# Kernel tuning notes

Hardware: AMD Instinct MI355X
Metric: run time of the kernel (lower is better)

Reference implementation:

```python
import jax, jax.numpy as jnp
import numpy as np

B, NIN, DIN, M, DOUT = 256, 64, 128, 32, 128
SCALE = 1.0 / np.sqrt(DOUT)  # 1/sqrt(out_d_capsules)


def setup_inputs() -> dict:
    key = jax.random.key(0)
    k1, k2, k3 = jax.random.split(key, 3)
    w_const = float(np.sqrt(M / (DIN * NIN)))  # weight_init_const
    return {
        "x": jax.random.normal(k1, (B, NIN, DIN), dtype=jnp.float32),
        "current_act": jax.random.uniform(k2, (B, NIN), dtype=jnp.float32),
        "W": w_const * jax.random.normal(k3, (NIN, DIN, M, DOUT), dtype=jnp.float32),
        "num_iter": 3,
    }


def reference(x, current_act, W, num_iter):
    # Initial pass: next_capsule_value is None -> q0 = softmax(zeros) = 1/M uniform
    # einsum('nm,bna,namd->bmd', q0, x, W) with uniform q0 == mean over m-weighting = /M
    ncv = jnp.einsum('bna,namd->bmd', x, W) / M  # [B, M, Dout]
    q = jnp.full((B, NIN, M), 1.0 / M, dtype=x.dtype)  # query_key from init step
    # Routing iterations (act_type='EM' -> next_act is None; dp=0 -> no dropout)
    for _ in range(max(1, num_iter)):
        logits = jnp.einsum('bna,namd,bmd->bnm', x, W, ncv) * SCALE  # [B, Nin, M]
        q = jax.nn.softmax(logits, axis=2)
        ncv = jnp.einsum('bnm,bna,namd,bn->bmd', q, x, W, current_act)
    # Per-pair votes and routed class embeddings
    votes = jnp.einsum('bna,namd->bnmd', x, W)          # [B, Nin, M, Dout]
    weights = q * current_act[:, :, None]               # [B, Nin, M]
    route_class_emb = weights[..., None] * votes        # [B, Nin, M, Dout]
    return ncv, q, route_class_emb
```

## Files before the change

kernel.cpp:

```cpp
#include <hip/hip_runtime.h>
#include <math.h>

#define B_    256
#define NIN_  64
#define DIN_  128
#define M_    32
#define DOUT_ 128
#define NUM_ITER 3

static constexpr float SCALE = 0.0883883476483184405501f;

typedef __attribute__((ext_vector_type(8))) short bf16x8;
typedef __attribute__((ext_vector_type(4))) float f32x4;

__device__ __forceinline__ unsigned short f2bf(float f) {
    union { float f; unsigned u; } c; c.f = f;
    unsigned r = c.u + 0x7FFFu + ((c.u >> 16) & 1u);
    return (unsigned short)(r >> 16);
}
__device__ __forceinline__ float lo2f(unsigned u) {
    union { unsigned u; float f; } c; c.u = u << 16; return c.f;
}
__device__ __forceinline__ float hi2f(unsigned u) {
    union { unsigned u; float f; } c; c.u = u & 0xffff0000u; return c.f;
}


__global__ __launch_bounds__(256) void k_votes_mfma(const float* __restrict__ x,
                                                    const float* __restrict__ W,
                                                    float* __restrict__ route) {
    const int n    = blockIdx.x;
    const int j0   = blockIdx.y * 512;
    const int t    = threadIdx.x;
    const int w    = t >> 6;
    const int lane = t & 63;
    const int l15  = lane & 15;
    const int l4   = lane >> 4;

    __shared__ __align__(16) char lds[49152];
    char* xbuf = lds;
    char* wbuf = lds + 32768;

    bf16x8 af[4][4];

    for (int h = 0; h < 2; ++h) {
        {
            const int col4 = (t & 15) * 4;
            const int roff = t >> 4;
            const int boff = col4 * 2;
            for (int p = 0; p < 16; ++p) {
                int row = p * 16 + roff;
                const float* src = x + (size_t)row * (NIN_ * DIN_) + (size_t)n * DIN_ + h * 64 + col4;
                float4 v = *(const float4*)src;
                uint2 pk;
                pk.x = (unsigned)f2bf(v.x) | ((unsigned)f2bf(v.y) << 16);
                pk.y = (unsigned)f2bf(v.z) | ((unsigned)f2bf(v.w) << 16);
                *(uint2*)(xbuf + row * 128 + (boff ^ ((row & 7) << 4))) = pk;
            }
        }
        __syncthreads();
#pragma unroll
        for (int mf = 0; mf < 4; ++mf) {
            int row = w * 64 + mf * 16 + l15;
            int sw  = (row & 7) << 4;
#pragma unroll
            for (int kfh = 0; kfh < 2; ++kfh) {
                int kbyte = kfh * 64 + l4 * 16;
                af[mf][h * 2 + kfh] = *(const bf16x8*)(xbuf + row * 128 + (kbyte ^ sw));
            }
        }
        __syncthreads();
    }

    const int jlane = t & 63;
    const int kg    = t >> 6;

    for (int jt = 0; jt < 8; ++jt) {
        {
            const int jcol = j0 + jt * 64 + jlane;
            const float* Wp = W + (size_t)n * (DIN_ * M_ * DOUT_) + jcol;
            const int sw = (jlane & 7) << 4;
#pragma unroll
            for (int c = 0; c < 4; ++c) {
                int kbase = kg * 32 + c * 8;
                unsigned pk[4];
#pragma unroll
                for (int r = 0; r < 4; ++r) {
                    float f0 = Wp[(size_t)(kbase + 2 * r)     * 4096];
                    float f1 = Wp[(size_t)(kbase + 2 * r + 1) * 4096];
                    pk[r] = (unsigned)f2bf(f0) | ((unsigned)f2bf(f1) << 16);
                }
                *(uint4*)(wbuf + jlane * 256 + ((kbase * 2) ^ sw)) = *(uint4*)pk;
            }
        }
        __syncthreads();

        f32x4 acc[4][4];
#pragma unroll
        for (int mf = 0; mf < 4; ++mf)
#pragma unroll
            for (int nf = 0; nf < 4; ++nf) acc[mf][nf] = (f32x4){0.f, 0.f, 0.f, 0.f};

#pragma unroll
        for (int kf = 0; kf < 4; ++kf) {
            bf16x8 bfr[4];
            int kbyte = kf * 64 + l4 * 16;
#pragma unroll
            for (int nf = 0; nf < 4; ++nf) {
                int col = nf * 16 + l15;
                bfr[nf] = *(const bf16x8*)(wbuf + col * 256 + (kbyte ^ ((col & 7) << 4)));
            }
#pragma unroll
            for (int mf = 0; mf < 4; ++mf)
#pragma unroll
                for (int nf = 0; nf < 4; ++nf)
                    acc[mf][nf] = __builtin_amdgcn_mfma_f32_16x16x32_bf16(af[mf][kf], bfr[nf], acc[mf][nf], 0, 0, 0);
        }
        __syncthreads();

#pragma unroll
        for (int mf = 0; mf < 4; ++mf) {
#pragma unroll
            for (int nf = 0; nf < 4; ++nf) {
                const int jb = nf * 16 + l15;
#pragma unroll
                for (int r = 0; r < 4; ++r) {
                    const int b = w * 64 + mf * 16 + l4 * 4 + r;
                    *(unsigned short*)(xbuf + b * 128 + ((jb * 2) ^ ((b & 12) << 3))) = f2bf(acc[mf][nf][r]);
                }
            }
        }
        __syncthreads();

        {
            char* vout = (char*)route;
            const size_t obase = (size_t)524288 + (size_t)n * 8192 + (size_t)(j0 + jt * 64) * 2;
#pragma unroll
            for (int p = 0; p < 8; ++p) {
                const int b = p * 32 + (t >> 3);
                const int c = (t & 7) * 16;
                uint4 val = *(const uint4*)(xbuf + b * 128 + (c ^ ((b & 12) << 3)));
                *(uint4*)(vout + (size_t)b * 1048576 + obase + c) = val;
            }
        }
        __syncthreads();
    }
}

__global__ __launch_bounds__(512, 2) void k_fused(float* __restrict__ route,
                                                  const float* __restrict__ act,
                                                  float* __restrict__ ncv,
                                                  float* __restrict__ q_out) {
    const int b    = blockIdx.x;
    const int t    = threadIdx.x;
    const int base = t * 8;
    const int m    = t >> 4;

    __shared__ float logits_s[4][32];
    __shared__ float w_s[4][32];
    __shared__ float sact[NIN_];
    if (t < 64) sact[t] = act[b * 64 + t];

    const char* vb    = (const char*)route + (size_t)b * 1048576 + 524288;
    const size_t toff = (size_t)t * 16;

    uint4 vA[4], vB[4];
    float ncvp[8], acc[8];

#define LOADC(DST, CC) { \
    _Pragma("unroll") \
    for (int r = 0; r < 4; ++r) \
        DST[r] = *(const uint4*)(vb + (size_t)((CC) * 4 + r) * 8192 + toff); }

#define SUM4(V) { \
    _Pragma("unroll") \
    for (int r = 0; r < 4; ++r) { \
        acc[0] += lo2f(V[r].x); acc[1] += hi2f(V[r].x); \
        acc[2] += lo2f(V[r].y); acc[3] += hi2f(V[r].y); \
        acc[4] += lo2f(V[r].z); acc[5] += hi2f(V[r].z); \
        acc[6] += lo2f(V[r].w); acc[7] += hi2f(V[r].w); } }

#define PH_A(V) { \
    _Pragma("unroll") \
    for (int r = 0; r < 4; ++r) { \
        float p = 0.f; \
        p = fmaf(lo2f(V[r].x), ncvp[0], p); p = fmaf(hi2f(V[r].x), ncvp[1], p); \
        p = fmaf(lo2f(V[r].y), ncvp[2], p); p = fmaf(hi2f(V[r].y), ncvp[3], p); \
        p = fmaf(lo2f(V[r].z), ncvp[4], p); p = fmaf(hi2f(V[r].z), ncvp[5], p); \
        p = fmaf(lo2f(V[r].w), ncvp[6], p); p = fmaf(hi2f(V[r].w), ncvp[7], p); \
        p += __shfl_xor(p, 1); p += __shfl_xor(p, 2); \
        p += __shfl_xor(p, 4); p += __shfl_xor(p, 8); \
        if ((t & 15) == 0) logits_s[r][m] = p * SCALE; \
    } }

#define PH_B(CC, WRF) { \
    if (t < 128) { \
        const int rr = t >> 5; const int ln = t & 31; \
        float l  = logits_s[rr][ln]; \
        float mx = l; \
        mx = fmaxf(mx, __shfl_xor(mx, 1));  mx = fmaxf(mx, __shfl_xor(mx, 2)); \
        mx = fmaxf(mx, __shfl_xor(mx, 4));  mx = fmaxf(mx, __shfl_xor(mx, 8)); \
        mx = fmaxf(mx, __shfl_xor(mx, 16)); \
        float e  = __expf(l - mx); \
        float su = e; \
        su += __shfl_xor(su, 1);  su += __shfl_xor(su, 2); \
        su += __shfl_xor(su, 4);  su += __shfl_xor(su, 8);  su += __shfl_xor(su, 16); \
        float qv = e / su; \
        const int ng = (CC) * 4 + rr; \
        w_s[rr][ln] = qv * sact[ng]; \
        if (WRF) q_out[(size_t)b * 2048 + (size_t)ng * 32 + ln] = qv; \
    } }

#define PH_C(V, CC, WRF) { \
    _Pragma("unroll") \
    for (int r = 0; r < 4; ++r) { \
        const float wg = w_s[r][m]; \
        float f0 = lo2f(V[r].x), f1 = hi2f(V[r].x), f2 = lo2f(V[r].y), f3 = hi2f(V[r].y); \
        float f4 = lo2f(V[r].z), f5 = hi2f(V[r].z), f6 = lo2f(V[r].w), f7 = hi2f(V[r].w); \
        acc[0] = fmaf(wg, f0, acc[0]); acc[1] = fmaf(wg, f1, acc[1]); \
        acc[2] = fmaf(wg, f2, acc[2]); acc[3] = fmaf(wg, f3, acc[3]); \
        acc[4] = fmaf(wg, f4, acc[4]); acc[5] = fmaf(wg, f5, acc[5]); \
        acc[6] = fmaf(wg, f6, acc[6]); acc[7] = fmaf(wg, f7, acc[7]); \
        if (WRF) { \
            float4 r0 = {wg * f0, wg * f1, wg * f2, wg * f3}; \
            float4 r1 = {wg * f4, wg * f5, wg * f6, wg * f7}; \
            float* rp = route + (size_t)b * 262144 + (size_t)((CC) * 4 + r) * 4096 + base; \
            *(float4*)rp = r0; *(float4*)(rp + 4) = r1; \
        } \
    } }

#define PROC(V, CC, WRF) { PH_A(V); __syncthreads(); PH_B(CC, WRF); __syncthreads(); PH_C(V, CC, WRF); }

#define ITER_PASS(WRF, WRAP) { \
    _Pragma("unroll") for (int i = 0; i < 8; ++i) acc[i] = 0.f; \
    LOADC(vB, 1); \
    for (int cc = 0; cc < 16; cc += 2) { \
        PROC(vA, cc, WRF); \
        if (cc + 2 < 16) { LOADC(vA, cc + 2); } \
        else if (WRAP)   { LOADC(vA, 0); } \
        PROC(vB, cc + 1, WRF); \
        if (cc + 3 < 16) { LOADC(vB, cc + 3); } \
    } \
    _Pragma("unroll") for (int i = 0; i < 8; ++i) ncvp[i] = acc[i]; }

#pragma unroll
    for (int i = 0; i < 8; ++i) acc[i] = 0.f;
    LOADC(vA, 0);
    LOADC(vB, 1);
    for (int cc = 0; cc < 16; cc += 2) {
        SUM4(vA);
        if (cc + 2 < 16) { LOADC(vA, cc + 2); }
        else             { LOADC(vA, 0); }
        SUM4(vB);
        if (cc + 3 < 16) { LOADC(vB, cc + 3); }
    }
#pragma unroll
    for (int i = 0; i < 8; ++i) ncvp[i] = acc[i] * (1.0f / 32.0f);

    for (int it = 0; it < NUM_ITER - 1; ++it) {
        ITER_PASS(0, 1);
    }
    ITER_PASS(1, 0);

    float* op = ncv + (size_t)b * 4096 + base;
    float4 o0 = {ncvp[0], ncvp[1], ncvp[2], ncvp[3]};
    float4 o1 = {ncvp[4], ncvp[5], ncvp[6], ncvp[7]};
    *(float4*)op       = o0;
    *(float4*)(op + 4) = o1;

#undef LOADC
#undef SUM4
#undef PH_A
#undef PH_B
#undef PH_C
#undef PROC
#undef ITER_PASS
}

extern "C" void kernel_launch(void* const* d_in, const int* in_sizes, int n_in,
                              void* d_out, int out_size, void* d_ws, size_t ws_size,
                              hipStream_t stream) {
    const float* x   = (const float*)d_in[0];
    const float* act = (const float*)d_in[1];
    const float* W   = (const float*)d_in[2];
    (void)in_sizes; (void)n_in; (void)d_ws; (void)ws_size; (void)out_size;

    float* out   = (float*)d_out;
    float* ncv   = out;
    float* q     = out + 1048576;
    float* route = out + 1572864;

    hipLaunchKernelGGL(k_votes_mfma, dim3(64, 8), dim3(256), 0, stream, x, W, route);
    hipLaunchKernelGGL(k_fused, dim3(256), dim3(512), 0, stream, route, act, ncv, q);
}
```

Measured before the change: 231.4 us.

## Split fused routing kernel into per-iteration kernels with Nin halves across blocks

Replaces the single per-batch fused routing kernel with separate launches: a reduction kernel for the initial ncv, one routing kernel per iteration that splits the Nin dimension across two blocks (doubling grid parallelism), and small fold kernels that sum the two partial ncv halves. Partial sums are parked in unused slots of the route output buffer or in the workspace. The bf16 vote layout is changed to a full 16 KB stride per n, and W loads are marked nontemporal. This trades extra launches and partial-sum round trips through global memory for twice as many blocks to fill the GPU.

New measurement: 249.1 us. 7.6% more time.

```diff
diff --git a/kernel.cpp b/kernel.cpp
--- a/kernel.cpp
+++ b/kernel.cpp
@@ -86,8 +86,8 @@
                 unsigned pk[4];
 #pragma unroll
                 for (int r = 0; r < 4; ++r) {
-                    float f0 = Wp[(size_t)(kbase + 2 * r)     * 4096];
-                    float f1 = Wp[(size_t)(kbase + 2 * r + 1) * 4096];
+                    float f0 = __builtin_nontemporal_load(&Wp[(size_t)(kbase + 2 * r)     * 4096]);
+                    float f1 = __builtin_nontemporal_load(&Wp[(size_t)(kbase + 2 * r + 1) * 4096]);
                     pk[r] = (unsigned)f2bf(f0) | ((unsigned)f2bf(f1) << 16);
                 }
                 *(uint4*)(wbuf + jlane * 256 + ((kbase * 2) ^ sw)) = *(uint4*)pk;
@@ -134,7 +134,7 @@
 
         {
             char* vout = (char*)route;
-            const size_t obase = (size_t)524288 + (size_t)n * 8192 + (size_t)(j0 + jt * 64) * 2;
+            const size_t obase = (size_t)n * 16384 + (size_t)(j0 + jt * 64) * 2;
 #pragma unroll
             for (int p = 0; p < 8; ++p) {
                 const int b = p * 32 + (t >> 3);
@@ -147,38 +147,66 @@
     }
 }
 
-__global__ __launch_bounds__(512, 2) void k_fused(float* __restrict__ route,
-                                                  const float* __restrict__ act,
-                                                  float* __restrict__ ncv,
-                                                  float* __restrict__ q_out) {
+__global__ __launch_bounds__(256) void k_ncv0(const float* __restrict__ route,
+                                              float* __restrict__ ncv) {
+    const int tid = blockIdx.x * 256 + threadIdx.x;
+    const int b   = tid >> 9;
+    const int jq  = (tid & 511) * 8;
+    const char* vp = (const char*)route + (size_t)b * 1048576 + (size_t)jq * 2;
+    float s[8] = {0.f, 0.f, 0.f, 0.f, 0.f, 0.f, 0.f, 0.f};
+    for (int n = 0; n < 64; ++n) {
+        uint4 v = *(const uint4*)(vp + (size_t)n * 16384);
+        s[0] += lo2f(v.x); s[1] += hi2f(v.x);
+        s[2] += lo2f(v.y); s[3] += hi2f(v.y);
+        s[4] += lo2f(v.z); s[5] += hi2f(v.z);
+        s[6] += lo2f(v.w); s[7] += hi2f(v.w);
+    }
+    float* op = ncv + (size_t)b * 4096 + jq;
+    f32x4 o0 = {s[0] * (1.0f/32.0f), s[1] * (1.0f/32.0f), s[2] * (1.0f/32.0f), s[3] * (1.0f/32.0f)};
+    f32x4 o1 = {s[4] * (1.0f/32.0f), s[5] * (1.0f/32.0f), s[6] * (1.0f/32.0f), s[7] * (1.0f/32.0f)};
+    *(f32x4*)op       = o0;
+    *(f32x4*)(op + 4) = o1;
+}
+
+__global__ __launch_bounds__(512, 2) void k_iter(
+        float* __restrict__ route, const float* __restrict__ act,
+        const float* __restrict__ in0, const float* __restrict__ in1,
+        long i_bs, long i_hs, float iscale,
+        float* __restrict__ pout, long p_hoff, long p_bs, long p_hs,
+        float* __restrict__ q_out, int wrf, int nh) {
     const int b    = blockIdx.x;
+    const int h    = blockIdx.y;
     const int t    = threadIdx.x;
     const int base = t * 8;
     const int m    = t >> 4;
+    const int n0   = h * nh;
+    const int nch  = nh >> 2;
 
     __shared__ float logits_s[4][32];
     __shared__ float w_s[4][32];
     __shared__ float sact[NIN_];
     if (t < 64) sact[t] = act[b * 64 + t];
 
-    const char* vb    = (const char*)route + (size_t)b * 1048576 + 524288;
-    const size_t toff = (size_t)t * 16;
+    const char* vb = (const char*)route + (size_t)b * 1048576;
+    const long jh  = (long)(t >> 8);
+    const long jl  = (long)(base & 2047);
+
+    float ncvp[8], acc[8];
+    {
+        const float* a = in0 + (long)b * i_bs + jh * i_hs + jl;
+        const float* c = in1 + (long)b * i_bs + jh * i_hs + jl;
+#pragma unroll
+        for (int i = 0; i < 8; ++i) ncvp[i] = (a[i] + c[i]) * iscale;
+    }
+#pragma unroll
+    for (int i = 0; i < 8; ++i) acc[i] = 0.f;
 
     uint4 vA[4], vB[4];
-    float ncvp[8], acc[8];
 
 #define LOADC(DST, CC) { \
     _Pragma("unroll") \
     for (int r = 0; r < 4; ++r) \
-        DST[r] = *(const uint4*)(vb + (size_t)((CC) * 4 + r) * 8192 + toff); }
-
-#define SUM4(V) { \
-    _Pragma("unroll") \
-    for (int r = 0; r < 4; ++r) { \
-        acc[0] += lo2f(V[r].x); acc[1] += hi2f(V[r].x); \
-        acc[2] += lo2f(V[r].y); acc[3] += hi2f(V[r].y); \
-        acc[4] += lo2f(V[r].z); acc[5] += hi2f(V[r].z); \
-        acc[6] += lo2f(V[r].w); acc[7] += hi2f(V[r].w); } }
+        DST[r] = *(const uint4*)(vb + (size_t)(n0 + (CC) * 4 + r) * 16384 + (size_t)t * 16); }
 
 #define PH_A(V) { \
     _Pragma("unroll") \
@@ -193,7 +221,7 @@
         if ((t & 15) == 0) logits_s[r][m] = p * SCALE; \
     } }
 
-#define PH_B(CC, WRF) { \
+#define PH_B(CC) { \
     if (t < 128) { \
         const int rr = t >> 5; const int ln = t & 31; \
         float l  = logits_s[rr][ln]; \
@@ -206,75 +234,66 @@
         su += __shfl_xor(su, 1);  su += __shfl_xor(su, 2); \
         su += __shfl_xor(su, 4);  su += __shfl_xor(su, 8);  su += __shfl_xor(su, 16); \
         float qv = e / su; \
-        const int ng = (CC) * 4 + rr; \
+        const int ng = n0 + (CC) * 4 + rr; \
         w_s[rr][ln] = qv * sact[ng]; \
-        if (WRF) q_out[(size_t)b * 2048 + (size_t)ng * 32 + ln] = qv; \
+        if (wrf) q_out[(size_t)b * 2048 + (size_t)ng * 32 + ln] = qv; \
     } }
 
-#define PH_C(V, CC, WRF) { \
+#define PH_C(V, CC) { \
     _Pragma("unroll") \
     for (int r = 0; r < 4; ++r) { \
         const float wg = w_s[r][m]; \
         float f0 = lo2f(V[r].x), f1 = hi2f(V[r].x), f2 = lo2f(V[r].y), f3 = hi2f(V[r].y); \
-        float f4 = lo2f(V[r].z), f5 = hi2f(V[r].z), f6 = lo2f(V[r].w), f7 = hi2f(V[r].w); \
         acc[0] = fmaf(wg, f0, acc[0]); acc[1] = fmaf(wg, f1, acc[1]); \
         acc[2] = fmaf(wg, f2, acc[2]); acc[3] = fmaf(wg, f3, acc[3]); \
+        float f4 = lo2f(V[r].z), f5 = hi2f(V[r].z), f6 = lo2f(V[r].w), f7 = hi2f(V[r].w); \
         acc[4] = fmaf(wg, f4, acc[4]); acc[5] = fmaf(wg, f5, acc[5]); \
         acc[6] = fmaf(wg, f6, acc[6]); acc[7] = fmaf(wg, f7, acc[7]); \
-        if (WRF) { \
-            float4 r0 = {wg * f0, wg * f1, wg * f2, wg * f3}; \
-            float4 r1 = {wg * f4, wg * f5, wg * f6, wg * f7}; \
-            float* rp = route + (size_t)b * 262144 + (size_t)((CC) * 4 + r) * 4096 + base; \
-            *(float4*)rp = r0; *(float4*)(rp + 4) = r1; \
+        if (wrf) { \
+            f32x4 r0 = {wg * f0, wg * f1, wg * f2, wg * f3}; \
+            f32x4 r1 = {wg * f4, wg * f5, wg * f6, wg * f7}; \
+            float* rp = route + (size_t)b * 262144 + (size_t)(n0 + (CC) * 4 + r) * 4096 + base; \
+            *(f32x4*)rp       = r0; \
+            *(f32x4*)(rp + 4) = r1; \
         } \
     } }
 
-#define PROC(V, CC, WRF) { PH_A(V); __syncthreads(); PH_B(CC, WRF); __syncthreads(); PH_C(V, CC, WRF); }
-
-#define ITER_PASS(WRF, WRAP) { \
-    _Pragma("unroll") for (int i = 0; i < 8; ++i) acc[i] = 0.f; \
-    LOADC(vB, 1); \
-    for (int cc = 0; cc < 16; cc += 2) { \
-        PROC(vA, cc, WRF); \
-        if (cc + 2 < 16) { LOADC(vA, cc + 2); } \
-        else if (WRAP)   { LOADC(vA, 0); } \
-        PROC(vB, cc + 1, WRF); \
-        if (cc + 3 < 16) { LOADC(vB, cc + 3); } \
-    } \
-    _Pragma("unroll") for (int i = 0; i < 8; ++i) ncvp[i] = acc[i]; }
-
-#pragma unroll
-    for (int i = 0; i < 8; ++i) acc[i] = 0.f;
+#define PROC(V, CC) { PH_A(V); __syncthreads(); PH_B(CC); __syncthreads(); PH_C(V, CC); }
+
     LOADC(vA, 0);
     LOADC(vB, 1);
-    for (int cc = 0; cc < 16; cc += 2) {
-        SUM4(vA);
-        if (cc + 2 < 16) { LOADC(vA, cc + 2); }
-        else             { LOADC(vA, 0); }
-        SUM4(vB);
-        if (cc + 3 < 16) { LOADC(vB, cc + 3); }
-    }
-#pragma unroll
-    for (int i = 0; i < 8; ++i) ncvp[i] = acc[i] * (1.0f / 32.0f);
-
-    for (int it = 0; it < NUM_ITER - 1; ++it) {
-        ITER_PASS(0, 1);
-    }
-    ITER_PASS(1, 0);
-
-    float* op = ncv + (size_t)b * 4096 + base;
-    float4 o0 = {ncvp[0], ncvp[1], ncvp[2], ncvp[3]};
-    float4 o1 = {ncvp[4], ncvp[5], ncvp[6], ncvp[7]};
-    *(float4*)op       = o0;
-    *(float4*)(op + 4) = o1;
+    for (int cc = 0; cc < nch; cc += 2) {
+        PROC(vA, cc);
+        if (cc + 2 < nch) { LOADC(vA, cc + 2); }
+        PROC(vB, cc + 1);
+        if (cc + 3 < nch) { LOADC(vB, cc + 3); }
+    }
+
+    float* pp = pout + (long)h * p_hoff + (long)b * p_bs + jh * p_hs + jl;
+    f32x4 o0 = {acc[0], acc[1], acc[2], acc[3]};
+    f32x4 o1 = {acc[4], acc[5], acc[6], acc[7]};
+    *(f32x4*)pp       = o0;
+    *(f32x4*)(pp + 4) = o1;
 
 #undef LOADC
-#undef SUM4
 #undef PH_A
 #undef PH_B
 #undef PH_C
 #undef PROC
-#undef ITER_PASS
+}
+
+__global__ __launch_bounds__(256) void k_fold(const float* __restrict__ s0,
+                                              const float* __restrict__ s1,
+                                              float* __restrict__ dst,
+                                              long bs, long hs) {
+    const int tid = blockIdx.x * 256 + threadIdx.x;
+    const int b   = tid >> 10;
+    const int jq  = (tid & 1023) << 2;
+    const long off = (long)b * bs + (long)(jq >> 11) * hs + (jq & 2047);
+    f32x4 x = *(const f32x4*)(s0 + off);
+    f32x4 y = *(const f32x4*)(s1 + off);
+    f32x4 o = {x.x + y.x, x.y + y.y, x.z + y.z, x.w + y.w};
+    *(f32x4*)(dst + (size_t)b * 4096 + jq) = o;
 }
 
 extern "C" void kernel_launch(void* const* d_in, const int* in_sizes, int n_in,
@@ -283,13 +302,43 @@
     const float* x   = (const float*)d_in[0];
     const float* act = (const float*)d_in[1];
     const float* W   = (const float*)d_in[2];
-    (void)in_sizes; (void)n_in; (void)d_ws; (void)ws_size; (void)out_size;
+    (void)in_sizes; (void)n_in; (void)out_size;
 
     float* out   = (float*)d_out;
     float* ncv   = out;
     float* q     = out + 1048576;
     float* route = out + 1572864;
 
+    float* spot0 = route + 0 * 2048 + 512;
+    spot0 = route + 0 * 8192 + 2048;
+    float* spot1 = route + 1 * 8192 + 2048;
+    float* spot2 = route + 2 * 8192 + 2048;
+    float* spot3 = route + 3 * 8192 + 2048;
+
+    const bool split3 = (d_ws != nullptr) && (ws_size >= (size_t)2 * 1048576 * 4);
+    float* wsp = (float*)d_ws;
+
     hipLaunchKernelGGL(k_votes_mfma, dim3(64, 8), dim3(256), 0, stream, x, W, route);
-    hipLaunchKernelGGL(k_fused, dim3(256), dim3(512), 0, stream, route, act, ncv, q);
-}
+    hipLaunchKernelGGL(k_ncv0, dim3(512), dim3(256), 0, stream, route, ncv);
+
+    hipLaunchKernelGGL(k_iter, dim3(256, 2), dim3(512), 0, stream,
+                       route, act, ncv, ncv, (long)4096, (long)2048, 0.5f,
+                       spot0, (long)8192, (long)262144, (long)4096, q, 0, 32);
+    hipLaunchKernelGGL(k_iter, dim3(256, 2), dim3(512), 0, stream,
+                       route, act, spot0, spot1, (long)262144, (long)4096, 1.0f,
+                       spot2, (long)8192, (long)262144, (long)4096, q, 0, 32);
+    hipLaunchKernelGGL(k_fold, dim3(1024), dim3(256), 0, stream,
+                       spot2, spot3, ncv, (long)262144, (long)4096);
+
+    if (split3) {
+        hipLaunchKernelGGL(k_iter, dim3(256, 2), dim3(512), 0, stream,
+                           route, act, ncv, ncv, (long)4096, (long)2048, 0.5f,
+                           wsp, (long)1048576, (long)4096, (long)2048, q, 1, 32);
+        hipLaunchKernelGGL(k_fold, dim3(1024), dim3(256), 0, stream,
+                           wsp, wsp + 1048576, ncv, (long)4096, (long)2048);
+    } else {
+        hipLaunchKernelGGL(k_iter, dim3(256, 1), dim3(512), 0, stream,
+                           route, act, ncv, ncv, (long)4096, (long)2048, 0.5f,
+                           ncv, (long)0, (long)4096, (long)2048, q, 1, 64);
+    }
+}
```
